# Kernel tuning notes

Hardware: AMD Instinct MI355X
Metric: run time of the kernel (lower is better)

Reference implementation:

```python
import jax, jax.numpy as jnp
import numpy as np
import math

B, T, H = 16, 2048, 128

def setup_inputs() -> dict:
    key = jax.random.key(0)
    kq, kk, kv = jax.random.split(key, 3)
    q = jax.random.normal(kq, (B, T, H), dtype=jnp.float32)
    k = jax.random.normal(kk, (B, T, H), dtype=jnp.float32)
    v = jax.random.normal(kv, (B, T, H), dtype=jnp.float32)
    # causal mask, shape (1,1,T,T) as in the torch module
    mask = jnp.tril(jnp.ones((T, T), dtype=jnp.int32))[None, None]
    return {"q": q, "k": k, "v": v, "mask": mask}

def reference(q, k, v, mask) -> jnp.ndarray:
    scale = math.sqrt(q.shape[-1])
    # (B,T,T) attention logits
    att = jnp.einsum("btd,bsd->bts", q, k) / scale
    m = mask[0, 0]  # (T,T), broadcasts over batch
    att = jnp.where(m == 0, -jnp.inf, att)
    att = jax.nn.softmax(att, axis=-1)
    # dropout is identity in eval mode (p=0.0)
    return jnp.einsum("bts,bsd->btd", att, v)
```

## Files before the change

### kernel.cpp

```cpp
#include <hip/hip_runtime.h>
#include <hip/hip_bf16.h>

#define TT 2048
#define DD 128
#define NB 16
#define NTILE 32
#define TILE_BYTES 16384

typedef __bf16 bf16x8 __attribute__((ext_vector_type(8)));
typedef __bf16 bf16x4 __attribute__((ext_vector_type(4)));
typedef float f32x4 __attribute__((ext_vector_type(4)));

#define GLOAD_LDS16(g, l) __builtin_amdgcn_global_load_lds( \
    (const __attribute__((address_space(1))) void*)(g),     \
    (__attribute__((address_space(3))) void*)(l), 16, 0, 0)

__device__ __forceinline__ float warp16_sum(float v) {
    v += __shfl_xor(v, 1);
    v += __shfl_xor(v, 2);
    v += __shfl_xor(v, 4);
    v += __shfl_xor(v, 8);
    return v;
}
__device__ __forceinline__ float bf2f(unsigned int u16) {
    union { unsigned int i; float f; } x; x.i = u16 << 16; return x.f;
}

__global__ __launch_bounds__(256) void prepass(
    const float* __restrict__ K, const float* __restrict__ V,
    char* __restrict__ KB, char* __restrict__ VTB)
{
    const int t = blockIdx.x;
    const int b = blockIdx.y;
    const int tid = threadIdx.x;
    const int kb = t * 64;
    char* kdst = KB  + (size_t)(b * NTILE + t) * TILE_BYTES;
    char* vdst = VTB + (size_t)(b * NTILE + t) * TILE_BYTES;
    const float* kp = K + ((size_t)b * TT + kb) * DD;
    const float* vp = V + ((size_t)b * TT + kb) * DD;

    #pragma unroll
    for (int it = 0; it < 4; ++it) {
        int key = it * 16 + (tid >> 4);
        int d0  = (tid & 15) * 8;
        const float4* s = (const float4*)(kp + (size_t)key * DD + d0);
        float4 f0 = s[0], f1 = s[1];
        bf16x8 h;
        h[0]=(__bf16)f0.x; h[1]=(__bf16)f0.y; h[2]=(__bf16)f0.z; h[3]=(__bf16)f0.w;
        h[4]=(__bf16)f1.x; h[5]=(__bf16)f1.y; h[6]=(__bf16)f1.z; h[7]=(__bf16)f1.w;
        *(bf16x8*)(kdst + key * 256 + ((d0 * 2) ^ ((key & 7) << 4))) = h;
    }
    #pragma unroll
    for (int it = 0; it < 4; ++it) {
        int d  = tid & 127;
        int k0 = ((tid >> 7) + it * 2) * 8;
        bf16x8 h;
        #pragma unroll
        for (int j = 0; j < 8; ++j)
            h[j] = (__bf16)vp[(size_t)(k0 + j) * DD + d];
        *(bf16x8*)(vdst + d * 128 + ((k0 * 2) ^ ((d & 7) << 4))) = h;
    }
}

__global__ __launch_bounds__(512, 4) void attn_main(
    const float* __restrict__ Q,
    const char* __restrict__ KB, const char* __restrict__ VTB,
    float* __restrict__ O, char* __restrict__ SLOTS,
    int CHUNK, int NCMAX, int QBMIN)
{
    __shared__ __align__(16) unsigned short Klds[2][64 * 128];
    __shared__ __align__(16) unsigned short Vs[2][128 * 64];
    __shared__ __align__(16) unsigned short Plds[8][16 * 64];

    const int b  = blockIdx.x;
    const int qb = 15 - blockIdx.y;
    const int ntile = 2 * qb + 2;
    const int t0 = blockIdx.z * CHUNK;
    if (t0 >= ntile) return;
    const int t1 = min(ntile, t0 + CHUNK);

    const int tid  = threadIdx.x;
    const int lane = tid & 63;
    const int w    = tid >> 6;
    const int x    = lane & 15;
    const int hi   = lane >> 4;
    const int qrow0 = qb * 128 + w * 16;

    const float SCALE = 0.08838834764831845f;

    const float* qp = Q + ((size_t)b * TT + qrow0) * DD;
    bf16x8 qf[4];
    #pragma unroll
    for (int kc = 0; kc < 4; ++kc) {
        const float4* s0 = (const float4*)(qp + x * DD + kc * 32 + 8 * hi);
        float4 f0 = s0[0], f1 = s0[1];
        bf16x8 t;
        t[0]=(__bf16)f0.x; t[1]=(__bf16)f0.y; t[2]=(__bf16)f0.z; t[3]=(__bf16)f0.w;
        t[4]=(__bf16)f1.x; t[5]=(__bf16)f1.y; t[6]=(__bf16)f1.z; t[7]=(__bf16)f1.w;
        qf[kc] = t;
    }

    f32x4 o[8];
    #pragma unroll
    for (int nt = 0; nt < 8; ++nt) o[nt] = (f32x4){0.f, 0.f, 0.f, 0.f};
    float lsum[4] = {0.f, 0.f, 0.f, 0.f};

    const char* kbase = KB  + (size_t)b * NTILE * TILE_BYTES;
    const char* vbase = VTB + (size_t)b * NTILE * TILE_BYTES;

    const int seg0 = w * 2;
    auto STAGE = [&](int t, int buf) {
        const char* ks = kbase + (size_t)t * TILE_BYTES;
        const char* vs = vbase + (size_t)t * TILE_BYTES;
        #pragma unroll
        for (int s = 0; s < 2; ++s) {
            int seg = seg0 + s;
            GLOAD_LDS16(ks + seg * 1024 + lane * 16, (char*)Klds[buf] + seg * 1024);
            GLOAD_LDS16(vs + seg * 1024 + lane * 16, (char*)Vs[buf]  + seg * 1024);
        }
    };

    STAGE(t0, 0);
    int cur = 0;
    char* pmine = (char*)Plds[w];

    for (int t = t0; t < t1; ++t) {
        const int kb = t * 64;
        __syncthreads();

        if (t + 1 < t1) STAGE(t + 1, cur ^ 1);

        const int ntm = (qrow0 + 15 - kb) >> 4;
        if (ntm >= 0) {
            const bool edge = (kb + 63 > qrow0);
            const int  ntmax = ntm > 3 ? 3 : ntm;
            const char* kb8 = (const char*)Klds[cur];
            float p[4][4];
            #pragma unroll
            for (int nt = 0; nt < 4; ++nt) {
                int key = nt * 16 + x;
                if (nt <= ntmax) {
                    f32x4 acc = (f32x4){0.f, 0.f, 0.f, 0.f};
                    #pragma unroll
                    for (int kc = 0; kc < 4; ++kc) {
                        int off = key * 256 + ((kc * 64 + 16 * hi) ^ ((key & 7) << 4));
                        bf16x8 bfr = *(const bf16x8*)(kb8 + off);
                        acc = __builtin_amdgcn_mfma_f32_16x16x32_bf16(qf[kc], bfr, acc, 0, 0, 0);
                    }
                    #pragma unroll
                    for (int r = 0; r < 4; ++r) {
                        bool msk = edge && (kb + key > qrow0 + 4 * hi + r);
                        float pe = msk ? 0.f : __expf(acc[r] * SCALE);
                        p[nt][r] = pe;
                        lsum[r] += pe;
                    }
                } else {
                    #pragma unroll
                    for (int r = 0; r < 4; ++r) p[nt][r] = 0.f;
                }
            }

            #pragma unroll
            for (int nt = 0; nt < 4; ++nt) {
                #pragma unroll
                for (int r = 0; r < 4; ++r) {
                    int q = 4 * hi + r;
                    int off = q * 128 + (((nt * 16 + x) * 2) ^ ((q & 7) << 4));
                    *(unsigned short*)(pmine + off) =
                        __builtin_bit_cast(unsigned short, (__bf16)p[nt][r]);
                }
            }

            const char* vb8 = (const char*)Vs[cur];
            #pragma unroll
            for (int kc = 0; kc < 2; ++kc) {
                bf16x8 af = *(const bf16x8*)(pmine + x * 128 + ((kc * 64 + 16 * hi) ^ ((x & 7) << 4)));
                #pragma unroll
                for (int nt = 0; nt < 8; ++nt) {
                    int d = nt * 16 + x;
                    bf16x8 bfr = *(const bf16x8*)(vb8 + d * 128 + ((kc * 64 + 16 * hi) ^ ((d & 7) << 4)));
                    o[nt] = __builtin_amdgcn_mfma_f32_16x16x32_bf16(af, bfr, o[nt], 0, 0, 0);
                }
            }
        }
        cur ^= 1;
    }

    float lr[4];
    #pragma unroll
    for (int r = 0; r < 4; ++r) lr[r] = warp16_sum(lsum[r]);

    if (t0 == 0 && t1 == ntile) {
        float* op = O + ((size_t)b * TT + qrow0) * DD;
        #pragma unroll
        for (int r = 0; r < 4; ++r) {
            float inv = 1.0f / lr[r];
            #pragma unroll
            for (int nt = 0; nt < 8; ++nt)
                op[(size_t)(4 * hi + r) * DD + nt * 16 + x] = o[nt][r] * inv;
        }
    } else {
        const int NQ = 16 - QBMIN;
        char* slot = SLOTS + (size_t)((b * NQ + (qb - QBMIN)) * NCMAX + blockIdx.z) * 33280;
        unsigned short* so = (unsigned short*)slot;
        float* sl = (float*)(slot + 32768);
        #pragma unroll
        for (int r = 0; r < 4; ++r) {
            int row = w * 16 + 4 * hi + r;
            #pragma unroll
            for (int nt = 0; nt < 8; ++nt)
                so[row * 128 + nt * 16 + x] =
                    __builtin_bit_cast(unsigned short, (__bf16)o[nt][r]);
            if (x == 0) sl[row] = lr[r];
        }
    }
}

__global__ __launch_bounds__(256) void attn_combine(
    const char* __restrict__ SLOTS, float* __restrict__ O,
    int CHUNK, int NCMAX, int QBMIN)
{
    const int qb = QBMIN + blockIdx.x;
    const int b  = blockIdx.y;
    const int nc = (2 * qb + 2 + CHUNK - 1) / CHUNK;
    const int NQ = 16 - QBMIN;
    const int row  = threadIdx.x >> 1;
    const int half = (threadIdx.x & 1) * 64;
    const char* base = SLOTS + (size_t)((b * NQ + (qb - QBMIN)) * NCMAX) * 33280;

    float l = 0.f;
    for (int c = 0; c < nc; ++c)
        l += *(const float*)(base + (size_t)c * 33280 + 32768 + row * 4);
    float inv = 1.0f / l;

    float* op = O + ((size_t)b * TT + qb * 128 + row) * DD + half;
    #pragma unroll
    for (int g = 0; g < 8; ++g) {
        f32x4 a0 = (f32x4){0.f,0.f,0.f,0.f}, a1 = (f32x4){0.f,0.f,0.f,0.f};
        for (int c = 0; c < nc; ++c) {
            const uint4 u = *(const uint4*)(base + (size_t)c * 33280 + row * 256 + half * 2 + g * 16);
            a0[0] += bf2f(u.x & 0xffffu); a0[1] += bf2f(u.x >> 16);
            a0[2] += bf2f(u.y & 0xffffu); a0[3] += bf2f(u.y >> 16);
            a1[0] += bf2f(u.z & 0xffffu); a1[1] += bf2f(u.z >> 16);
            a1[2] += bf2f(u.w & 0xffffu); a1[3] += bf2f(u.w >> 16);
        }
        float4 r0, r1;
        r0.x=a0[0]*inv; r0.y=a0[1]*inv; r0.z=a0[2]*inv; r0.w=a0[3]*inv;
        r1.x=a1[0]*inv; r1.y=a1[1]*inv; r1.z=a1[2]*inv; r1.w=a1[3]*inv;
        *(float4*)(op + g * 8)     = r0;
        *(float4*)(op + g * 8 + 4) = r1;
    }
}

__global__ __launch_bounds__(256) void attn_fb(
    const float* __restrict__ Q, const float* __restrict__ K,
    const float* __restrict__ V, float* __restrict__ O)
{
    __shared__ __align__(16) unsigned short Klds[2][64 * 128];
    __shared__ __align__(16) unsigned short Vsh[2][128 * 64];
    __shared__ __align__(16) unsigned short Plds[4][16 * 64];

    const int qb = 31 - blockIdx.x;
    const int b  = blockIdx.y;
    const int ntile = qb + 1;
    const int tid  = threadIdx.x;
    const int lane = tid & 63;
    const int w    = tid >> 6;
    const int x    = lane & 15;
    const int hi   = lane >> 4;
    const int qrow0 = qb * 64 + w * 16;

    const float* qp    = Q + ((size_t)b * TT + qrow0) * DD;
    const float* kbase = K + (size_t)b * TT * DD;
    const float* vbase = V + (size_t)b * TT * DD;
    const float SCALE = 0.08838834764831845f;

    const int krow = tid >> 5;
    const int d4   = (tid & 31) * 4;
    const int dd   = tid & 127;
    const int g    = tid >> 7;

    bf16x8 qf[4];
    #pragma unroll
    for (int kc = 0; kc < 4; ++kc) {
        const float4* s0 = (const float4*)(qp + x * DD + kc * 32 + 8 * hi);
        float4 f0 = s0[0], f1 = s0[1];
        bf16x8 t;
        t[0]=(__bf16)f0.x; t[1]=(__bf16)f0.y; t[2]=(__bf16)f0.z; t[3]=(__bf16)f0.w;
        t[4]=(__bf16)f1.x; t[5]=(__bf16)f1.y; t[6]=(__bf16)f1.z; t[7]=(__bf16)f1.w;
        qf[kc] = t;
    }
    f32x4 o[8];
    #pragma unroll
    for (int nt = 0; nt < 8; ++nt) o[nt] = (f32x4){0.f,0.f,0.f,0.f};
    float lsum[4] = {0.f,0.f,0.f,0.f};
    float4 kreg[8];
    float  vreg[32];

    auto LOAD = [&](int t) {
        const float* kp = kbase + (size_t)(t * 64) * DD;
        const float* vp = vbase + (size_t)(t * 64) * DD;
        #pragma unroll
        for (int it = 0; it < 8; ++it)
            kreg[it] = *(const float4*)(kp + (size_t)(it * 8 + krow) * DD + d4);
        #pragma unroll
        for (int j = 0; j < 32; ++j)
            vreg[j] = vp[(size_t)(g * 32 + j) * DD + dd];
    };
    auto WRITE = [&](int buf) {
        char* kb8 = (char*)Klds[buf];
        #pragma unroll
        for (int it = 0; it < 8; ++it) {
            int key = it * 8 + krow;
            float4 f = kreg[it];
            bf16x4 h;
            h[0]=(__bf16)f.x; h[1]=(__bf16)f.y; h[2]=(__bf16)f.z; h[3]=(__bf16)f.w;
            *(bf16x4*)(kb8 + key * 256 + ((d4 * 2) ^ ((key & 7) << 4))) = h;
        }
        char* vb8 = (char*)Vsh[buf];
        #pragma unroll
        for (int m4 = 0; m4 < 4; ++m4) {
            bf16x8 h;
            #pragma unroll
            for (int j = 0; j < 8; ++j) h[j] = (__bf16)vreg[m4 * 8 + j];
            *(bf16x8*)(vb8 + dd * 128 + ((g * 64 + m4 * 16) ^ ((dd & 7) << 4))) = h;
        }
    };

    LOAD(0); WRITE(0);
    int cur = 0;
    char* pmine = (char*)Plds[w];

    for (int t = 0; t < ntile; ++t) {
        const int kb = t * 64;
        __syncthreads();
        if (t + 1 < ntile) LOAD(t + 1);

        const bool diag  = (t == qb);
        const int  ntmax = diag ? w : 3;
        const char* kb8  = (const char*)Klds[cur];
        float p[4][4];
        #pragma unroll
        for (int nt = 0; nt < 4; ++nt) {
            int key = nt * 16 + x;
            if (nt <= ntmax) {
                f32x4 acc = (f32x4){0.f,0.f,0.f,0.f};
                #pragma unroll
                for (int kc = 0; kc < 4; ++kc) {
                    int off = key * 256 + ((kc * 64 + 16 * hi) ^ ((key & 7) << 4));
                    bf16x8 bfr = *(const bf16x8*)(kb8 + off);
                    acc = __builtin_amdgcn_mfma_f32_16x16x32_bf16(qf[kc], bfr, acc, 0, 0, 0);
                }
                #pragma unroll
                for (int r = 0; r < 4; ++r) {
                    bool msk = diag && (kb + key > qrow0 + 4 * hi + r);
                    float pe = msk ? 0.f : __expf(acc[r] * SCALE);
                    p[nt][r] = pe;
                    lsum[r] += pe;
                }
            } else {
                #pragma unroll
                for (int r = 0; r < 4; ++r) p[nt][r] = 0.f;
            }
        }
        #pragma unroll
        for (int nt = 0; nt < 4; ++nt)
            #pragma unroll
            for (int r = 0; r < 4; ++r) {
                int q = 4 * hi + r;
                *(unsigned short*)(pmine + q * 128 + (((nt * 16 + x) * 2) ^ ((q & 7) << 4))) =
                    __builtin_bit_cast(unsigned short, (__bf16)p[nt][r]);
            }
        const char* vb8 = (const char*)Vsh[cur];
        #pragma unroll
        for (int kc = 0; kc < 2; ++kc) {
            bf16x8 af = *(const bf16x8*)(pmine + x * 128 + ((kc * 64 + 16 * hi) ^ ((x & 7) << 4)));
            #pragma unroll
            for (int nt = 0; nt < 8; ++nt) {
                int d = nt * 16 + x;
                bf16x8 bfr = *(const bf16x8*)(vb8 + d * 128 + ((kc * 64 + 16 * hi) ^ ((d & 7) << 4)));
                o[nt] = __builtin_amdgcn_mfma_f32_16x16x32_bf16(af, bfr, o[nt], 0, 0, 0);
            }
        }
        if (t + 1 < ntile) WRITE(cur ^ 1);
        cur ^= 1;
    }
    float* op = O + ((size_t)b * TT + qrow0) * DD;
    #pragma unroll
    for (int r = 0; r < 4; ++r) {
        float lr = warp16_sum(lsum[r]);
        float inv = 1.0f / lr;
        #pragma unroll
        for (int nt = 0; nt < 8; ++nt)
            op[(size_t)(4 * hi + r) * DD + nt * 16 + x] = o[nt][r] * inv;
    }
}

extern "C" void kernel_launch(void* const* d_in, const int* in_sizes, int n_in,
                              void* d_out, int out_size, void* d_ws, size_t ws_size,
                              hipStream_t stream) {
    const float* q = (const float*)d_in[0];
    const float* k = (const float*)d_in[1];
    const float* v = (const float*)d_in[2];
    float* out = (float*)d_out;

    const size_t PRE = (size_t)2 * NB * NTILE * TILE_BYTES;
    auto slotsNeed = [](int QBMIN, int NCMAX) {
        return (size_t)(16 - QBMIN) * NB * NCMAX * 33280;
    };

    char* kb  = (char*)d_ws;
    char* vtb = kb + (size_t)NB * NTILE * TILE_BYTES;
    char* slots = vtb + (size_t)NB * NTILE * TILE_BYTES;

    if (ws_size >= PRE + slotsNeed(4, 4)) {
        prepass<<<dim3(NTILE, NB), 256, 0, stream>>>(k, v, kb, vtb);
        attn_main<<<dim3(NB, 16, 4), 512, 0, stream>>>(q, kb, vtb, out, slots, 8, 4, 4);
        attn_combine<<<dim3(12, NB), 256, 0, stream>>>(slots, out, 8, 4, 4);
    } else if (ws_size >= PRE + slotsNeed(8, 2)) {
        prepass<<<dim3(NTILE, NB), 256, 0, stream>>>(k, v, kb, vtb);
        attn_main<<<dim3(NB, 16, 2), 512, 0, stream>>>(q, kb, vtb, out, slots, 16, 2, 8);
        attn_combine<<<dim3(8, NB), 256, 0, stream>>>(slots, out, 16, 2, 8);
    } else if (ws_size >= PRE) {
        prepass<<<dim3(NTILE, NB), 256, 0, stream>>>(k, v, kb, vtb);
        attn_main<<<dim3(NB, 16, 1), 512, 0, stream>>>(q, kb, vtb, out, slots, 32, 1, 16);
    } else {
        attn_fb<<<dim3(32, NB), 256, 0, stream>>>(q, k, v, out);
    }
}
```

Measured before the change: 74.80 us.

## Switch attention main loop to 32x32x16 MFMA with register-resident P

Rewrites the main attention kernel to use 32x32x16 bf16 MFMAs with 4 waves of 32 query rows each, computing S transposed so the probabilities can be packed into A-fragments with a cross-half shuffle. This removes the per-wave LDS round-trip for P. The prepass K/V swizzles are changed to match the new fragment layout. Chunks are now split evenly across the z dimension. Costs include higher register pressure (f32x16 accumulators, 8 Q fragments) at launch_bounds(256,2) and fewer threads per block.

```diff
diff --git a/kernel.cpp b/kernel.cpp
--- a/kernel.cpp
+++ b/kernel.cpp
@@ -10,6 +10,7 @@
 typedef __bf16 bf16x8 __attribute__((ext_vector_type(8)));
 typedef __bf16 bf16x4 __attribute__((ext_vector_type(4)));
 typedef float f32x4 __attribute__((ext_vector_type(4)));
+typedef float f32x16 __attribute__((ext_vector_type(16)));
 
 #define GLOAD_LDS16(g, l) __builtin_amdgcn_global_load_lds( \
     (const __attribute__((address_space(1))) void*)(g),     \
@@ -24,6 +25,22 @@
 }
 __device__ __forceinline__ float bf2f(unsigned int u16) {
     union { unsigned int i; float f; } x; x.i = u16 << 16; return x.f;
+}
+__device__ __forceinline__ unsigned int pk2(float lo, float hi) {
+    unsigned short a = __builtin_bit_cast(unsigned short, (__bf16)lo);
+    unsigned short b = __builtin_bit_cast(unsigned short, (__bf16)hi);
+    return (unsigned int)a | ((unsigned int)b << 16);
+}
+__device__ __forceinline__ bf16x8 frag4(unsigned int a, unsigned int b,
+                                        unsigned int c, unsigned int d) {
+    uint4 u = make_uint4(a, b, c, d);
+    return __builtin_bit_cast(bf16x8, u);
+}
+__device__ __forceinline__ f32x16 z16() {
+    f32x16 v;
+    #pragma unroll
+    for (int i = 0; i < 16; ++i) v[i] = 0.f;
+    return v;
 }
 
 __global__ __launch_bounds__(256) void prepass(
@@ -33,11 +50,10 @@
     const int t = blockIdx.x;
     const int b = blockIdx.y;
     const int tid = threadIdx.x;
-    const int kb = t * 64;
     char* kdst = KB  + (size_t)(b * NTILE + t) * TILE_BYTES;
     char* vdst = VTB + (size_t)(b * NTILE + t) * TILE_BYTES;
-    const float* kp = K + ((size_t)b * TT + kb) * DD;
-    const float* vp = V + ((size_t)b * TT + kb) * DD;
+    const float* kp = K + ((size_t)b * TT + t * 64) * DD;
+    const float* vp = V + ((size_t)b * TT + t * 64) * DD;
 
     #pragma unroll
     for (int it = 0; it < 4; ++it) {
@@ -48,7 +64,7 @@
         bf16x8 h;
         h[0]=(__bf16)f0.x; h[1]=(__bf16)f0.y; h[2]=(__bf16)f0.z; h[3]=(__bf16)f0.w;
         h[4]=(__bf16)f1.x; h[5]=(__bf16)f1.y; h[6]=(__bf16)f1.z; h[7]=(__bf16)f1.w;
-        *(bf16x8*)(kdst + key * 256 + ((d0 * 2) ^ ((key & 7) << 4))) = h;
+        *(bf16x8*)(kdst + key * 256 + ((d0 * 2) ^ ((key & 15) << 4))) = h;
     }
     #pragma unroll
     for (int it = 0; it < 4; ++it) {
@@ -58,71 +74,71 @@
         #pragma unroll
         for (int j = 0; j < 8; ++j)
             h[j] = (__bf16)vp[(size_t)(k0 + j) * DD + d];
-        *(bf16x8*)(vdst + d * 128 + ((k0 * 2) ^ ((d & 7) << 4))) = h;
-    }
-}
-
-__global__ __launch_bounds__(512, 4) void attn_main(
+        *(bf16x8*)(vdst + (d >> 1) * 256 +
+                   ((((d & 1) * 128) + 2 * k0) ^ (((d >> 1) & 15) << 4))) = h;
+    }
+}
+
+__global__ __launch_bounds__(256, 2) void attn_main(
     const float* __restrict__ Q,
     const char* __restrict__ KB, const char* __restrict__ VTB,
     float* __restrict__ O, char* __restrict__ SLOTS,
     int CHUNK, int NCMAX, int QBMIN)
 {
-    __shared__ __align__(16) unsigned short Klds[2][64 * 128];
-    __shared__ __align__(16) unsigned short Vs[2][128 * 64];
-    __shared__ __align__(16) unsigned short Plds[8][16 * 64];
+    __shared__ __align__(16) unsigned short Klds[2][8192];
+    __shared__ __align__(16) unsigned short Vs[2][8192];
 
     const int b  = blockIdx.x;
     const int qb = 15 - blockIdx.y;
     const int ntile = 2 * qb + 2;
-    const int t0 = blockIdx.z * CHUNK;
-    if (t0 >= ntile) return;
-    const int t1 = min(ntile, t0 + CHUNK);
+    const int nc = (ntile + CHUNK - 1) / CHUNK;
+    if ((int)blockIdx.z >= nc) return;
+    const int t0 = (int)(((long)blockIdx.z * ntile) / nc);
+    const int t1 = (int)(((long)(blockIdx.z + 1) * ntile) / nc);
 
     const int tid  = threadIdx.x;
     const int lane = tid & 63;
     const int w    = tid >> 6;
-    const int x    = lane & 15;
-    const int hi   = lane >> 4;
-    const int qrow0 = qb * 128 + w * 16;
+    const int ln   = lane & 31;
+    const int hi   = lane >> 5;
+    const int qrow0 = qb * 128 + w * 32;
+    const int q_abs = qrow0 + ln;
 
     const float SCALE = 0.08838834764831845f;
 
-    const float* qp = Q + ((size_t)b * TT + qrow0) * DD;
-    bf16x8 qf[4];
-    #pragma unroll
-    for (int kc = 0; kc < 4; ++kc) {
-        const float4* s0 = (const float4*)(qp + x * DD + kc * 32 + 8 * hi);
-        float4 f0 = s0[0], f1 = s0[1];
+    const float* qrow = Q + ((size_t)b * TT + q_abs) * DD + 8 * hi;
+    bf16x8 qf[8];
+    #pragma unroll
+    for (int kc = 0; kc < 8; ++kc) {
+        float4 f0 = *(const float4*)(qrow + kc * 16);
+        float4 f1 = *(const float4*)(qrow + kc * 16 + 4);
         bf16x8 t;
         t[0]=(__bf16)f0.x; t[1]=(__bf16)f0.y; t[2]=(__bf16)f0.z; t[3]=(__bf16)f0.w;
         t[4]=(__bf16)f1.x; t[5]=(__bf16)f1.y; t[6]=(__bf16)f1.z; t[7]=(__bf16)f1.w;
         qf[kc] = t;
     }
 
-    f32x4 o[8];
-    #pragma unroll
-    for (int nt = 0; nt < 8; ++nt) o[nt] = (f32x4){0.f, 0.f, 0.f, 0.f};
-    float lsum[4] = {0.f, 0.f, 0.f, 0.f};
+    f32x16 o[4];
+    #pragma unroll
+    for (int dg = 0; dg < 4; ++dg) o[dg] = z16();
+    float lsum = 0.f;
 
     const char* kbase = KB  + (size_t)b * NTILE * TILE_BYTES;
     const char* vbase = VTB + (size_t)b * NTILE * TILE_BYTES;
 
-    const int seg0 = w * 2;
     auto STAGE = [&](int t, int buf) {
         const char* ks = kbase + (size_t)t * TILE_BYTES;
         const char* vs = vbase + (size_t)t * TILE_BYTES;
         #pragma unroll
-        for (int s = 0; s < 2; ++s) {
-            int seg = seg0 + s;
-            GLOAD_LDS16(ks + seg * 1024 + lane * 16, (char*)Klds[buf] + seg * 1024);
-            GLOAD_LDS16(vs + seg * 1024 + lane * 16, (char*)Vs[buf]  + seg * 1024);
+        for (int j = 0; j < 4; ++j) {
+            int off = (w * 4 + j) * 1024 + lane * 16;
+            GLOAD_LDS16(ks + off, (char*)Klds[buf] + off);
+            GLOAD_LDS16(vs + off, (char*)Vs[buf]  + off);
         }
     };
 
     STAGE(t0, 0);
     int cur = 0;
-    char* pmine = (char*)Plds[w];
 
     for (int t = t0; t < t1; ++t) {
         const int kb = t * 64;
@@ -130,74 +146,73 @@
 
         if (t + 1 < t1) STAGE(t + 1, cur ^ 1);
 
-        const int ntm = (qrow0 + 15 - kb) >> 4;
-        if (ntm >= 0) {
+        if (kb <= qrow0 + 31) {
             const bool edge = (kb + 63 > qrow0);
-            const int  ntmax = ntm > 3 ? 3 : ntm;
-            const char* kb8 = (const char*)Klds[cur];
-            float p[4][4];
+            const char* kl = (const char*)Klds[cur];
+            const char* vl = (const char*)Vs[cur];
+
+            auto PROC = [&](int kg) {
+                const int key = kg * 32 + ln;
+                const int swk = (key & 15) << 4;
+                const char* krow = kl + key * 256;
+                f32x16 a0 = z16(), a1 = z16();
+                #pragma unroll
+                for (int kc = 0; kc < 8; kc += 2) {
+                    bf16x8 kf0 = *(const bf16x8*)(krow + ((kc * 32 + 16 * hi) ^ swk));
+                    bf16x8 kf1 = *(const bf16x8*)(krow + (((kc + 1) * 32 + 16 * hi) ^ swk));
+                    a0 = __builtin_amdgcn_mfma_f32_32x32x16_bf16(kf0, qf[kc],     a0, 0, 0, 0);
+                    a1 = __builtin_amdgcn_mfma_f32_32x32x16_bf16(kf1, qf[kc + 1], a1, 0, 0, 0);
+                }
+                float p[16];
+                #pragma unroll
+                for (int reg = 0; reg < 16; ++reg) {
+                    int key_abs = kb + kg * 32 + (reg & 3) + 8 * (reg >> 2) + 4 * hi;
+                    float pe = __expf((a0[reg] + a1[reg]) * SCALE);
+                    if (edge && key_abs > q_abs) pe = 0.f;
+                    p[reg] = pe;
+                    lsum += pe;
+                }
+                unsigned int wd[8], xr[8];
+                #pragma unroll
+                for (int i = 0; i < 8; ++i) wd[i] = pk2(p[2 * i], p[2 * i + 1]);
+                #pragma unroll
+                for (int i = 0; i < 8; ++i) xr[i] = __shfl_xor(wd[i], 32);
+                bf16x8 pa0 = hi ? frag4(xr[2], xr[3], wd[2], wd[3])
+                                : frag4(wd[0], wd[1], xr[0], xr[1]);
+                bf16x8 pa1 = hi ? frag4(xr[6], xr[7], wd[6], wd[7])
+                                : frag4(wd[4], wd[5], xr[4], xr[5]);
+                const int kc0 = 2 * kg;
+                #pragma unroll
+                for (int dg = 0; dg < 4; ++dg) {
+                    int d = dg * 32 + ln;
+                    const char* vrow = vl + (d >> 1) * 256;
+                    int hv = (d & 1) * 128;
+                    int swv = ((d >> 1) & 15) << 4;
+                    bf16x8 vf0 = *(const bf16x8*)(vrow + ((hv + kc0 * 32 + 16 * hi) ^ swv));
+                    bf16x8 vf1 = *(const bf16x8*)(vrow + ((hv + (kc0 + 1) * 32 + 16 * hi) ^ swv));
+                    o[dg] = __builtin_amdgcn_mfma_f32_32x32x16_bf16(pa0, vf0, o[dg], 0, 0, 0);
+                    o[dg] = __builtin_amdgcn_mfma_f32_32x32x16_bf16(pa1, vf1, o[dg], 0, 0, 0);
+                }
+            };
+
+            PROC(0);
+            if (kb + 32 <= qrow0 + 31) PROC(1);
+        }
+        cur ^= 1;
+    }
+
+    const float ltot = lsum + __shfl_xor(lsum, 32);
+
+    if (t0 == 0 && t1 == ntile) {
+        const float inv = 1.0f / ltot;
+        float* op = O + ((size_t)b * TT + qrow0) * DD;
+        #pragma unroll
+        for (int reg = 0; reg < 16; ++reg) {
+            int qr = (reg & 3) + 8 * (reg >> 2) + 4 * hi;
+            float iv = __shfl(inv, qr);
             #pragma unroll
-            for (int nt = 0; nt < 4; ++nt) {
-                int key = nt * 16 + x;
-                if (nt <= ntmax) {
-                    f32x4 acc = (f32x4){0.f, 0.f, 0.f, 0.f};
-                    #pragma unroll
-                    for (int kc = 0; kc < 4; ++kc) {
-                        int off = key * 256 + ((kc * 64 + 16 * hi) ^ ((key & 7) << 4));
-                        bf16x8 bfr = *(const bf16x8*)(kb8 + off);
-                        acc = __builtin_amdgcn_mfma_f32_16x16x32_bf16(qf[kc], bfr, acc, 0, 0, 0);
-                    }
-                    #pragma unroll
-                    for (int r = 0; r < 4; ++r) {
-                        bool msk = edge && (kb + key > qrow0 + 4 * hi + r);
-                        float pe = msk ? 0.f : __expf(acc[r] * SCALE);
-                        p[nt][r] = pe;
-                        lsum[r] += pe;
-                    }
-                } else {
-                    #pragma unroll
-                    for (int r = 0; r < 4; ++r) p[nt][r] = 0.f;
-                }
-            }
-
-            #pragma unroll
-            for (int nt = 0; nt < 4; ++nt) {
-                #pragma unroll
-                for (int r = 0; r < 4; ++r) {
-                    int q = 4 * hi + r;
-                    int off = q * 128 + (((nt * 16 + x) * 2) ^ ((q & 7) << 4));
-                    *(unsigned short*)(pmine + off) =
-                        __builtin_bit_cast(unsigned short, (__bf16)p[nt][r]);
-                }
-            }
-
-            const char* vb8 = (const char*)Vs[cur];
-            #pragma unroll
-            for (int kc = 0; kc < 2; ++kc) {
-                bf16x8 af = *(const bf16x8*)(pmine + x * 128 + ((kc * 64 + 16 * hi) ^ ((x & 7) << 4)));
-                #pragma unroll
-                for (int nt = 0; nt < 8; ++nt) {
-                    int d = nt * 16 + x;
-                    bf16x8 bfr = *(const bf16x8*)(vb8 + d * 128 + ((kc * 64 + 16 * hi) ^ ((d & 7) << 4)));
-                    o[nt] = __builtin_amdgcn_mfma_f32_16x16x32_bf16(af, bfr, o[nt], 0, 0, 0);
-                }
-            }
-        }
-        cur ^= 1;
-    }
-
-    float lr[4];
-    #pragma unroll
-    for (int r = 0; r < 4; ++r) lr[r] = warp16_sum(lsum[r]);
-
-    if (t0 == 0 && t1 == ntile) {
-        float* op = O + ((size_t)b * TT + qrow0) * DD;
-        #pragma unroll
-        for (int r = 0; r < 4; ++r) {
-            float inv = 1.0f / lr[r];
-            #pragma unroll
-            for (int nt = 0; nt < 8; ++nt)
-                op[(size_t)(4 * hi + r) * DD + nt * 16 + x] = o[nt][r] * inv;
+            for (int dg = 0; dg < 4; ++dg)
+                op[(size_t)qr * DD + dg * 32 + ln] = o[dg][reg] * iv;
         }
     } else {
         const int NQ = 16 - QBMIN;
@@ -205,14 +220,14 @@
         unsigned short* so = (unsigned short*)slot;
         float* sl = (float*)(slot + 32768);
         #pragma unroll
-        for (int r = 0; r < 4; ++r) {
-            int row = w * 16 + 4 * hi + r;
+        for (int reg = 0; reg < 16; ++reg) {
+            int row = w * 32 + (reg & 3) + 8 * (reg >> 2) + 4 * hi;
             #pragma unroll
-            for (int nt = 0; nt < 8; ++nt)
-                so[row * 128 + nt * 16 + x] =
-                    __builtin_bit_cast(unsigned short, (__bf16)o[nt][r]);
-            if (x == 0) sl[row] = lr[r];
-        }
+            for (int dg = 0; dg < 4; ++dg)
+                so[row * 128 + dg * 32 + ln] =
+                    __builtin_bit_cast(unsigned short, (__bf16)o[dg][reg]);
+        }
+        if (hi == 0) sl[w * 32 + ln] = ltot;
     }
 }
 
@@ -415,15 +430,15 @@
 
     if (ws_size >= PRE + slotsNeed(4, 4)) {
         prepass<<<dim3(NTILE, NB), 256, 0, stream>>>(k, v, kb, vtb);
-        attn_main<<<dim3(NB, 16, 4), 512, 0, stream>>>(q, kb, vtb, out, slots, 8, 4, 4);
+        attn_main<<<dim3(NB, 16, 4), 256, 0, stream>>>(q, kb, vtb, out, slots, 8, 4, 4);
         attn_combine<<<dim3(12, NB), 256, 0, stream>>>(slots, out, 8, 4, 4);
     } else if (ws_size >= PRE + slotsNeed(8, 2)) {
         prepass<<<dim3(NTILE, NB), 256, 0, stream>>>(k, v, kb, vtb);
-        attn_main<<<dim3(NB, 16, 2), 512, 0, stream>>>(q, kb, vtb, out, slots, 16, 2, 8);
+        attn_main<<<dim3(NB, 16, 2), 256, 0, stream>>>(q, kb, vtb, out, slots, 16, 2, 8);
         attn_combine<<<dim3(8, NB), 256, 0, stream>>>(slots, out, 16, 2, 8);
     } else if (ws_size >= PRE) {
         prepass<<<dim3(NTILE, NB), 256, 0, stream>>>(k, v, kb, vtb);
-        attn_main<<<dim3(NB, 16, 1), 512, 0, stream>>>(q, kb, vtb, out, slots, 32, 1, 16);
+        attn_main<<<dim3(NB, 16, 1), 256, 0, stream>>>(q, kb, vtb, out, slots, 32, 1, 16);
     } else {
         attn_fb<<<dim3(32, NB), 256, 0, stream>>>(q, k, v, out);
     }
```

After: 76.04 us. No clear change (+1.7%).
